# Kernel optimization log

Measured on AMD Instinct MI355X. Metric: run time of the kernel, lower is better.

## Reference

```python
import jax, jax.numpy as jnp
import numpy as np

NUM_EMB = 512
LATENT = 128
TEXT_DIM = 512


def setup_inputs() -> dict:
    key = jax.random.key(0)
    ks = jax.random.split(key, 12)
    B, N = 64, 8192
    x = jax.random.normal(ks[0], (B, N, 3), dtype=jnp.float32)
    s = jax.random.normal(ks[1], (B, N), dtype=jnp.float32)
    e = jax.random.normal(ks[2], (B, TEXT_DIM), dtype=jnp.float32)
    # point_mlp: Linear(4,64) -> ReLU -> Linear(64,128); weights stored (in,out)
    W1 = jax.random.normal(ks[3], (4, 64), dtype=jnp.float32) * 0.5
    b1 = jnp.zeros((64,), dtype=jnp.float32)
    W2 = jax.random.normal(ks[4], (64, 128), dtype=jnp.float32) * 0.125
    b2 = jnp.zeros((128,), dtype=jnp.float32)
    # latent_mlp: Linear(128+512,256) -> ReLU -> Linear(256,128)
    W3 = jax.random.normal(ks[5], (128 + TEXT_DIM, 256), dtype=jnp.float32) * 0.04
    b3 = jnp.zeros((256,), dtype=jnp.float32)
    W4 = jax.random.normal(ks[6], (256, LATENT), dtype=jnp.float32) * 0.0625
    b4 = jnp.zeros((LATENT,), dtype=jnp.float32)
    # codebook init uniform(-1/K, 1/K) as in torch code
    codebook = jax.random.uniform(ks[7], (NUM_EMB, LATENT), dtype=jnp.float32,
                                  minval=-1.0 / NUM_EMB, maxval=1.0 / NUM_EMB)
    return {"x": x, "s": s, "e": e, "W1": W1, "b1": b1, "W2": W2, "b2": b2,
            "W3": W3, "b3": b3, "W4": W4, "b4": b4, "codebook": codebook}


def reference(x, s, e, W1, b1, W2, b2, W3, b3, W4, b4, codebook):
    # PointNet feature extraction
    point_inp = jnp.concatenate([x, s[..., None]], axis=-1)        # (B,N,4)
    h = jax.nn.relu(point_inp @ W1 + b1)                           # (B,N,64)
    point_feat = h @ W2 + b2                                       # (B,N,128)
    global_feat = jnp.max(point_feat, axis=1)                      # (B,128)
    combined = jnp.concatenate([global_feat, e], axis=-1)          # (B,640)
    z_e = jax.nn.relu(combined @ W3 + b3) @ W4 + b4                # (B,latent)
    # VQ: squared-L2 distances to codebook, argmin, gather
    dists = (jnp.sum(z_e * z_e, axis=1, keepdims=True)
             - 2.0 * (z_e @ codebook.T)
             + jnp.sum(codebook * codebook, axis=1))               # (B,K)
    indices = jnp.argmin(dists, axis=1)                            # (B,)
    z_q = codebook[indices]                                        # (B,latent)
    sg = jax.lax.stop_gradient
    codebook_loss = jnp.mean((z_q - sg(z_e)) ** 2)
    commitment_loss = jnp.mean((z_e - sg(z_q)) ** 2)
    z_q_st = z_e + sg(z_q - z_e)
    return (z_q_st, z_e, codebook_loss, commitment_loss, indices)
```

## Files before the change

### kernel.cpp

```cpp
#include <hip/hip_runtime.h>

typedef unsigned int u32;
typedef __attribute__((ext_vector_type(4))) unsigned int u32x4;
typedef __attribute__((ext_vector_type(8))) short s16x8;
typedef __attribute__((ext_vector_type(16))) float f32x16;
typedef __attribute__((ext_vector_type(4))) float f32x4;

__device__ __forceinline__ u32 mono(float f) {
    u32 u = __float_as_uint(f);
    return (u & 0x80000000u) ? ~u : (u | 0x80000000u);
}
__device__ __forceinline__ float unmono(u32 k) {
    return __uint_as_float((k & 0x80000000u) ? (k & 0x7fffffffu) : ~k);
}
__device__ __forceinline__ u32 rne_hi(float a) {
    u32 u = __float_as_uint(a);
    return (u + 0x7FFFu + ((u >> 16) & 1u)) & 0xFFFF0000u;
}

__global__ void k0_init(u32* __restrict__ keys) {
    int idx = blockIdx.x * 256 + threadIdx.x;
    if (idx < 8192) keys[idx] = 0u;
}

__global__ __launch_bounds__(256, 4) void k1_pointfeat(
    const float* __restrict__ x, const float* __restrict__ s,
    const float* __restrict__ W1, const float* __restrict__ b1,
    const float* __restrict__ W2, u32* __restrict__ keys)
{
    __shared__ __align__(16) u32 Hlds[2 * 2 * 64 * 36];
    const int tid   = threadIdx.x;
    const int lane  = tid & 63;
    const int point = tid & 63;
    const int kq    = __builtin_amdgcn_readfirstlane(tid >> 6);
    const int cl    = lane & 31;
    const int kg    = lane >> 5;

    const int p0 = blockIdx.x * 512;
    const int b  = blockIdx.x >> 4;

    s16x8 wh[4], wl[4];
    #pragma unroll
    for (int sl = 0; sl < 4; ++sl)
        #pragma unroll
        for (int j = 0; j < 8; ++j) {
            float f = W2[(sl * 16 + kg * 8 + j) * 128 + kq * 32 + cl];
            u32 hb = rne_hi(f);
            float lo = f - __uint_as_float(hb);
            u32 lb = rne_hi(lo);
            wh[sl][j] = (short)(hb >> 16);
            wl[sl][j] = (short)(lb >> 16);
        }

    float rmax = -3.402823466e38f;

    #pragma unroll 1
    for (int g = 0; g < 8; ++g) {
        {
            const int gp = p0 + g * 64 + point;
            const float px = x[(size_t)gp * 3 + 0];
            const float py = x[(size_t)gp * 3 + 1];
            const float pz = x[(size_t)gp * 3 + 2];
            const float pw = s[gp];
            u32* Hw = &Hlds[(g & 1) * 4608 + point * 36 + kq * 8];
            #pragma unroll
            for (int h = 0; h < 2; ++h) {
                u32 hp[4], lp[4];
                #pragma unroll
                for (int c = 0; c < 4; ++c) {
                    const int k0 = kq * 16 + h * 8 + c * 2;
                    float a0 = fmaf(px, W1[k0],
                               fmaf(py, W1[64 + k0],
                               fmaf(pz, W1[128 + k0],
                               fmaf(pw, W1[192 + k0], b1[k0]))));
                    float a1 = fmaf(px, W1[k0 + 1],
                               fmaf(py, W1[65 + k0],
                               fmaf(pz, W1[129 + k0],
                               fmaf(pw, W1[193 + k0], b1[k0 + 1]))));
                    a0 = a0 > 0.f ? a0 : 0.f;
                    a1 = a1 > 0.f ? a1 : 0.f;
                    u32 h0 = rne_hi(a0), h1 = rne_hi(a1);
                    float l0 = a0 - __uint_as_float(h0);
                    float l1 = a1 - __uint_as_float(h1);
                    hp[c] = __builtin_amdgcn_perm(h1, h0, 0x07060302u);
                    lp[c] = __builtin_amdgcn_perm(__float_as_uint(l1),
                                                  __float_as_uint(l0), 0x07060302u);
                }
                u32x4 vh = {hp[0], hp[1], hp[2], hp[3]};
                u32x4 vl = {lp[0], lp[1], lp[2], lp[3]};
                *(u32x4*)(Hw + h * 4)        = vh;
                *(u32x4*)(Hw + 2304 + h * 4) = vl;
            }
        }
        __syncthreads();
        const u32* Hb = &Hlds[(g & 1) * 4608];
        f32x16 acc0 = {}, acc1 = {};
        __builtin_amdgcn_s_setprio(1);
        #pragma unroll
        for (int sl = 0; sl < 4; ++sl) {
            s16x8 ahi0 = *(const s16x8*)(Hb + cl * 36 + sl * 8 + kg * 4);
            s16x8 alo0 = *(const s16x8*)(Hb + 2304 + cl * 36 + sl * 8 + kg * 4);
            acc0 = __builtin_amdgcn_mfma_f32_32x32x16_bf16(ahi0, wh[sl], acc0, 0, 0, 0);
            acc0 = __builtin_amdgcn_mfma_f32_32x32x16_bf16(ahi0, wl[sl], acc0, 0, 0, 0);
            acc0 = __builtin_amdgcn_mfma_f32_32x32x16_bf16(alo0, wh[sl], acc0, 0, 0, 0);
            s16x8 ahi1 = *(const s16x8*)(Hb + (32 + cl) * 36 + sl * 8 + kg * 4);
            s16x8 alo1 = *(const s16x8*)(Hb + 2304 + (32 + cl) * 36 + sl * 8 + kg * 4);
            acc1 = __builtin_amdgcn_mfma_f32_32x32x16_bf16(ahi1, wh[sl], acc1, 0, 0, 0);
            acc1 = __builtin_amdgcn_mfma_f32_32x32x16_bf16(ahi1, wl[sl], acc1, 0, 0, 0);
            acc1 = __builtin_amdgcn_mfma_f32_32x32x16_bf16(alo1, wh[sl], acc1, 0, 0, 0);
        }
        __builtin_amdgcn_s_setprio(0);
        #pragma unroll
        for (int r = 0; r < 16; ++r)
            rmax = fmaxf(rmax, fmaxf(acc0[r], acc1[r]));
    }

    rmax = fmaxf(rmax, __shfl_xor(rmax, 32, 64));
    if (lane < 32)
        atomicMax(&keys[b * 128 + kq * 32 + cl], mono(rmax));
}

__global__ __launch_bounds__(256) void k2a_hidden(
    const u32* __restrict__ keys, const float* __restrict__ b2,
    const float* __restrict__ e,
    const float* __restrict__ W3, const float* __restrict__ b3,
    float* __restrict__ ws_hid)
{
    const int blk = blockIdx.x;
    const int b   = blk >> 2;
    const int c   = blk & 3;
    const int tid = threadIdx.x;
    const int u   = tid & 63;
    const int part = tid >> 6;
    __shared__ float comb[640];
    __shared__ float psum[4][64];

    for (int i = tid; i < 640; i += 256)
        comb[i] = (i < 128) ? unmono(keys[b * 128 + i]) + b2[i]
                            : e[b * 512 + (i - 128)];
    __syncthreads();

    const int gu = c * 64 + u;
    const float* __restrict__ Wp = W3 + (size_t)(part * 160) * 256 + gu;
    const float* __restrict__ cp = comb + part * 160;
    float a = 0.f;
    for (int i = 0; i < 160; ++i) a = fmaf(cp[i], Wp[(size_t)i * 256], a);
    psum[part][u] = a;
    __syncthreads();
    if (tid < 64) {
        float hv = psum[0][u] + psum[1][u] + psum[2][u] + psum[3][u] + b3[gu];
        ws_hid[b * 256 + gu] = hv > 0.f ? hv : 0.f;
    }
}

__global__ __launch_bounds__(512) void k2b_vq(
    const float* __restrict__ ws_hid,
    const float* __restrict__ W4, const float* __restrict__ b4,
    const float* __restrict__ cb, float* __restrict__ out,
    float* __restrict__ ws_loss)
{
    const int b = blockIdx.x, tid = threadIdx.x;
    __shared__ float hid[256];
    __shared__ float psum[4][128];
    __shared__ float ze[128];
    __shared__ float red_d[512];
    __shared__ int   red_i[512];
    __shared__ float lred[128];
    __shared__ float zzs;

    if (tid < 256) hid[tid] = ws_hid[b * 256 + tid];
    __syncthreads();

    {
        const int u = tid & 127, part = tid >> 7;
        const float* __restrict__ Wp = W4 + (size_t)(part * 64) * 128 + u;
        const float* __restrict__ hp = hid + part * 64;
        float a = 0.f;
        for (int i = 0; i < 64; ++i) a = fmaf(hp[i], Wp[(size_t)i * 128], a);
        psum[part][u] = a;
    }
    __syncthreads();
    if (tid < 128) {
        float a = psum[0][tid] + psum[1][tid] + psum[2][tid] + psum[3][tid] + b4[tid];
        ze[tid] = a;
        out[8192 + b * 128 + tid] = a;
    }
    __syncthreads();

    if (tid < 64) {
        float t = ze[tid] * ze[tid] + ze[tid + 64] * ze[tid + 64];
        #pragma unroll
        for (int d = 1; d < 64; d <<= 1) t += __shfl_xor(t, d, 64);
        if (tid == 0) zzs = t;
    }
    __syncthreads();

    {
        float dot = 0.f, cc = 0.f;
        const f32x4* __restrict__ cp = (const f32x4*)(cb + (size_t)tid * 128);
        for (int k4 = 0; k4 < 32; ++k4) {
            f32x4 v = cp[k4];
            dot = fmaf(ze[k4 * 4 + 0], v.x, dot);
            cc  = fmaf(v.x, v.x, cc);
            dot = fmaf(ze[k4 * 4 + 1], v.y, dot);
            cc  = fmaf(v.y, v.y, cc);
            dot = fmaf(ze[k4 * 4 + 2], v.z, dot);
            cc  = fmaf(v.z, v.z, cc);
            dot = fmaf(ze[k4 * 4 + 3], v.w, dot);
            cc  = fmaf(v.w, v.w, cc);
        }
        red_d[tid] = zzs - 2.f * dot + cc;
        red_i[tid] = tid;
    }
    __syncthreads();

    for (int sft = 256; sft >= 1; sft >>= 1) {
        if (tid < sft) {
            float da = red_d[tid], db = red_d[tid + sft];
            int   ia = red_i[tid], ib = red_i[tid + sft];
            if (db < da || (db == da && ib < ia)) { red_d[tid] = db; red_i[tid] = ib; }
        }
        __syncthreads();
    }
    const int bc = red_i[0];

    if (tid < 128) {
        float zq  = cb[(size_t)bc * 128 + tid];
        float zev = ze[tid];
        out[b * 128 + tid] = zev + (zq - zev);
        float d = zq - zev;
        lred[tid] = d * d;
    }
    if (tid == 0) out[16386 + b] = (float)bc;
    __syncthreads();
    if (tid < 64) {
        float t = lred[tid] + lred[tid + 64];
        #pragma unroll
        for (int d = 1; d < 64; d <<= 1) t += __shfl_xor(t, d, 64);
        if (tid == 0) ws_loss[b] = t;
    }
}

__global__ void k3_loss(const float* __restrict__ ws_loss, float* __restrict__ out)
{
    const int t = threadIdx.x;
    float v = ws_loss[t];
    #pragma unroll
    for (int d = 1; d < 64; d <<= 1) v += __shfl_xor(v, d, 64);
    if (t == 0) {
        float m = v / 8192.f;
        out[16384] = m;
        out[16385] = m;
    }
}

extern "C" void kernel_launch(void* const* d_in, const int* in_sizes, int n_in,
                              void* d_out, int out_size, void* d_ws, size_t ws_size,
                              hipStream_t stream) {
    const float* x  = (const float*)d_in[0];
    const float* s  = (const float*)d_in[1];
    const float* e  = (const float*)d_in[2];
    const float* W1 = (const float*)d_in[3];
    const float* b1 = (const float*)d_in[4];
    const float* W2 = (const float*)d_in[5];
    const float* b2 = (const float*)d_in[6];
    const float* W3 = (const float*)d_in[7];
    const float* b3 = (const float*)d_in[8];
    const float* W4 = (const float*)d_in[9];
    const float* b4 = (const float*)d_in[10];
    const float* cb = (const float*)d_in[11];
    float* out = (float*)d_out;

    u32*   keys    = (u32*)d_ws;
    float* ws_loss = (float*)d_ws + 8192;
    float* ws_hid  = (float*)d_ws + 8192 + 64;

    k0_init<<<32, 256, 0, stream>>>(keys);
    k1_pointfeat<<<1024, 256, 0, stream>>>(x, s, W1, b1, W2, keys);
    k2a_hidden<<<256, 256, 0, stream>>>(keys, b2, e, W3, b3, ws_hid);
    k2b_vq<<<64, 512, 0, stream>>>(ws_hid, W4, b4, cb, out, ws_loss);
    k3_loss<<<1, 64, 0, stream>>>(ws_loss, out);
}
```

Baseline: 54.29 us.

## Software-pipeline point staging and replace atomic max with per-block partials

The point-feature kernel now stages the next group's hidden activations into the alternate LDS buffer after issuing the current group's MFMAs, and prefetches the following group's point coordinates into registers, so global loads and VALU staging overlap with matrix work. The atomicMax on monotonic keys is replaced by per-block partial maxima written to workspace, which the hidden-layer kernel reduces over 16 partials. This removes the init kernel launch and the atomics, in exchange for extra workspace and a small reduction in k2a. Register pressure rises from holding prefetched coordinates.

```diff
diff --git a/kernel.cpp b/kernel.cpp
--- a/kernel.cpp
+++ b/kernel.cpp
@@ -6,27 +6,15 @@
 typedef __attribute__((ext_vector_type(16))) float f32x16;
 typedef __attribute__((ext_vector_type(4))) float f32x4;
 
-__device__ __forceinline__ u32 mono(float f) {
-    u32 u = __float_as_uint(f);
-    return (u & 0x80000000u) ? ~u : (u | 0x80000000u);
-}
-__device__ __forceinline__ float unmono(u32 k) {
-    return __uint_as_float((k & 0x80000000u) ? (k & 0x7fffffffu) : ~k);
-}
 __device__ __forceinline__ u32 rne_hi(float a) {
     u32 u = __float_as_uint(a);
     return (u + 0x7FFFu + ((u >> 16) & 1u)) & 0xFFFF0000u;
 }
 
-__global__ void k0_init(u32* __restrict__ keys) {
-    int idx = blockIdx.x * 256 + threadIdx.x;
-    if (idx < 8192) keys[idx] = 0u;
-}
-
 __global__ __launch_bounds__(256, 4) void k1_pointfeat(
     const float* __restrict__ x, const float* __restrict__ s,
     const float* __restrict__ W1, const float* __restrict__ b1,
-    const float* __restrict__ W2, u32* __restrict__ keys)
+    const float* __restrict__ W2, float* __restrict__ ws_part)
 {
     __shared__ __align__(16) u32 Hlds[2 * 2 * 64 * 36];
     const int tid   = threadIdx.x;
@@ -37,7 +25,6 @@
     const int kg    = lane >> 5;
 
     const int p0 = blockIdx.x * 512;
-    const int b  = blockIdx.x >> 4;
 
     s16x8 wh[4], wl[4];
     #pragma unroll
@@ -54,44 +41,54 @@
 
     float rmax = -3.402823466e38f;
 
+#define STAGE_GROUP(GG, PX, PY, PZ, PW)                                        \
+    {                                                                          \
+        u32* Hw = &Hlds[((GG) & 1) * 4608 + point * 36 + kq * 8];              \
+        _Pragma("unroll")                                                      \
+        for (int h = 0; h < 2; ++h) {                                          \
+            u32 hp[4], lp[4];                                                  \
+            _Pragma("unroll")                                                  \
+            for (int c = 0; c < 4; ++c) {                                      \
+                const int k0 = kq * 16 + h * 8 + c * 2;                        \
+                float a0 = fmaf(PX, W1[k0],                                    \
+                           fmaf(PY, W1[64 + k0],                               \
+                           fmaf(PZ, W1[128 + k0],                              \
+                           fmaf(PW, W1[192 + k0], b1[k0]))));                  \
+                float a1 = fmaf(PX, W1[k0 + 1],                                \
+                           fmaf(PY, W1[65 + k0],                               \
+                           fmaf(PZ, W1[129 + k0],                              \
+                           fmaf(PW, W1[193 + k0], b1[k0 + 1]))));              \
+                a0 = a0 > 0.f ? a0 : 0.f;                                      \
+                a1 = a1 > 0.f ? a1 : 0.f;                                      \
+                u32 h0 = rne_hi(a0), h1 = rne_hi(a1);                          \
+                float l0 = a0 - __uint_as_float(h0);                           \
+                float l1 = a1 - __uint_as_float(h1);                           \
+                hp[c] = __builtin_amdgcn_perm(h1, h0, 0x07060302u);            \
+                lp[c] = __builtin_amdgcn_perm(__float_as_uint(l1),             \
+                                              __float_as_uint(l0), 0x07060302u);\
+            }                                                                  \
+            u32x4 vh = {hp[0], hp[1], hp[2], hp[3]};                           \
+            u32x4 vl = {lp[0], lp[1], lp[2], lp[3]};                           \
+            *(u32x4*)(Hw + h * 4)        = vh;                                 \
+            *(u32x4*)(Hw + 2304 + h * 4) = vl;                                 \
+        }                                                                      \
+    }
+
+    {
+        const int gp = p0 + point;
+        float px = x[(size_t)gp * 3 + 0], py = x[(size_t)gp * 3 + 1];
+        float pz = x[(size_t)gp * 3 + 2], pw = s[gp];
+        STAGE_GROUP(0, px, py, pz, pw)
+    }
+    float pxn, pyn, pzn, pwn;
+    {
+        const int gp = p0 + 64 + point;
+        pxn = x[(size_t)gp * 3 + 0]; pyn = x[(size_t)gp * 3 + 1];
+        pzn = x[(size_t)gp * 3 + 2]; pwn = s[gp];
+    }
+
     #pragma unroll 1
     for (int g = 0; g < 8; ++g) {
-        {
-            const int gp = p0 + g * 64 + point;
-            const float px = x[(size_t)gp * 3 + 0];
-            const float py = x[(size_t)gp * 3 + 1];
-            const float pz = x[(size_t)gp * 3 + 2];
-            const float pw = s[gp];
-            u32* Hw = &Hlds[(g & 1) * 4608 + point * 36 + kq * 8];
-            #pragma unroll
-            for (int h = 0; h < 2; ++h) {
-                u32 hp[4], lp[4];
-                #pragma unroll
-                for (int c = 0; c < 4; ++c) {
-                    const int k0 = kq * 16 + h * 8 + c * 2;
-                    float a0 = fmaf(px, W1[k0],
-                               fmaf(py, W1[64 + k0],
-                               fmaf(pz, W1[128 + k0],
-                               fmaf(pw, W1[192 + k0], b1[k0]))));
-                    float a1 = fmaf(px, W1[k0 + 1],
-                               fmaf(py, W1[65 + k0],
-                               fmaf(pz, W1[129 + k0],
-                               fmaf(pw, W1[193 + k0], b1[k0 + 1]))));
-                    a0 = a0 > 0.f ? a0 : 0.f;
-                    a1 = a1 > 0.f ? a1 : 0.f;
-                    u32 h0 = rne_hi(a0), h1 = rne_hi(a1);
-                    float l0 = a0 - __uint_as_float(h0);
-                    float l1 = a1 - __uint_as_float(h1);
-                    hp[c] = __builtin_amdgcn_perm(h1, h0, 0x07060302u);
-                    lp[c] = __builtin_amdgcn_perm(__float_as_uint(l1),
-                                                  __float_as_uint(l0), 0x07060302u);
-                }
-                u32x4 vh = {hp[0], hp[1], hp[2], hp[3]};
-                u32x4 vl = {lp[0], lp[1], lp[2], lp[3]};
-                *(u32x4*)(Hw + h * 4)        = vh;
-                *(u32x4*)(Hw + 2304 + h * 4) = vl;
-            }
-        }
         __syncthreads();
         const u32* Hb = &Hlds[(g & 1) * 4608];
         f32x16 acc0 = {}, acc1 = {};
@@ -110,18 +107,27 @@
             acc1 = __builtin_amdgcn_mfma_f32_32x32x16_bf16(alo1, wh[sl], acc1, 0, 0, 0);
         }
         __builtin_amdgcn_s_setprio(0);
+        if (g < 7) {
+            STAGE_GROUP(g + 1, pxn, pyn, pzn, pwn)
+            if (g < 6) {
+                const int gp = p0 + (g + 2) * 64 + point;
+                pxn = x[(size_t)gp * 3 + 0]; pyn = x[(size_t)gp * 3 + 1];
+                pzn = x[(size_t)gp * 3 + 2]; pwn = s[gp];
+            }
+        }
         #pragma unroll
         for (int r = 0; r < 16; ++r)
             rmax = fmaxf(rmax, fmaxf(acc0[r], acc1[r]));
     }
+#undef STAGE_GROUP
 
     rmax = fmaxf(rmax, __shfl_xor(rmax, 32, 64));
     if (lane < 32)
-        atomicMax(&keys[b * 128 + kq * 32 + cl], mono(rmax));
+        ws_part[blockIdx.x * 128 + kq * 32 + cl] = rmax;
 }
 
 __global__ __launch_bounds__(256) void k2a_hidden(
-    const u32* __restrict__ keys, const float* __restrict__ b2,
+    const float* __restrict__ ws_part, const float* __restrict__ b2,
     const float* __restrict__ e,
     const float* __restrict__ W3, const float* __restrict__ b3,
     float* __restrict__ ws_hid)
@@ -135,9 +141,19 @@
     __shared__ float comb[640];
     __shared__ float psum[4][64];
 
-    for (int i = tid; i < 640; i += 256)
-        comb[i] = (i < 128) ? unmono(keys[b * 128 + i]) + b2[i]
-                            : e[b * 512 + (i - 128)];
+    for (int i = tid; i < 640; i += 256) {
+        float v;
+        if (i < 128) {
+            const float* __restrict__ pp = ws_part + (size_t)b * 16 * 128 + i;
+            float m = pp[0];
+            #pragma unroll
+            for (int t = 1; t < 16; ++t) m = fmaxf(m, pp[t * 128]);
+            v = m + b2[i];
+        } else {
+            v = e[b * 512 + (i - 128)];
+        }
+        comb[i] = v;
+    }
     __syncthreads();
 
     const int gu = c * 64 + u;
@@ -271,13 +287,12 @@
     const float* cb = (const float*)d_in[11];
     float* out = (float*)d_out;
 
-    u32*   keys    = (u32*)d_ws;
-    float* ws_loss = (float*)d_ws + 8192;
-    float* ws_hid  = (float*)d_ws + 8192 + 64;
-
-    k0_init<<<32, 256, 0, stream>>>(keys);
-    k1_pointfeat<<<1024, 256, 0, stream>>>(x, s, W1, b1, W2, keys);
-    k2a_hidden<<<256, 256, 0, stream>>>(keys, b2, e, W3, b3, ws_hid);
+    float* ws_part = (float*)d_ws;
+    float* ws_hid  = (float*)d_ws + 1024 * 128;
+    float* ws_loss = (float*)d_ws + 1024 * 128 + 64 * 256;
+
+    k1_pointfeat<<<1024, 256, 0, stream>>>(x, s, W1, b1, W2, ws_part);
+    k2a_hidden<<<256, 256, 0, stream>>>(ws_part, b2, e, W3, b3, ws_hid);
     k2b_vq<<<64, 512, 0, stream>>>(ws_hid, W4, b4, cb, out, ws_loss);
     k3_loss<<<1, 64, 0, stream>>>(ws_loss, out);
 }
```

Result: faster. 50.99 us (-6.1%).
